# Performance work log

Hardware: AMD Instinct MI355X
Metric: run time of the kernel (lower is better)

## Reference

```python
import jax, jax.numpy as jnp
import numpy as np

INPUT_DIM = 512
D_KQ = 64
D_V = 64
SEQ = 8192


def setup_inputs() -> dict:
    key = jax.random.key(0)
    k_x, k_q, k_k, k_v = jax.random.split(key, 4)
    x = jax.random.normal(k_x, (SEQ, INPUT_DIM), dtype=jnp.float32)
    # Original uses torch.rand (uniform [0,1)) for the parameters.
    W_query = jax.random.uniform(k_q, (INPUT_DIM, D_KQ), dtype=jnp.float32)
    W_key = jax.random.uniform(k_k, (INPUT_DIM, D_KQ), dtype=jnp.float32)
    W_value = jax.random.uniform(k_v, (INPUT_DIM, D_V), dtype=jnp.float32)
    return {"x": x, "W_query": W_query, "W_key": W_key, "W_value": W_value}


def reference(x, W_query, W_key, W_value):
    # Full-recompute path of AttentionOptimized: single-head attention.
    Q = x @ W_query          # [T, d_kq]
    K = x @ W_key            # [T, d_kq]
    V = x @ W_value          # [T, d_v]
    scale = jnp.asarray(D_KQ, x.dtype) ** 0.5
    scores = Q @ K.T         # [T, T]
    attn = jax.nn.softmax(scores / scale, axis=-1)
    return attn @ V          # [T, d_v]
```

## Files before the change

kernel.cpp:

```cpp
#include <hip/hip_runtime.h>
#include <hip/hip_bf16.h>
#include <math.h>

#define SEQ 8192
#define DIN 512
#define DH  64
#define SG  8
#define CHUNK (SEQ / SG)
#define BK  64
#define NIT (CHUNK / BK)
#define LDK 64
#define SXP 516

typedef float f32x4 __attribute__((ext_vector_type(4)));
typedef short short8 __attribute__((ext_vector_type(8)));
typedef ushort us4 __attribute__((ext_vector_type(4)));

static __device__ __forceinline__ ushort bf16_of(float v) {
  __hip_bfloat16 h = __float2bfloat16(v);
  return *reinterpret_cast<ushort*>(&h);
}
static __device__ __forceinline__ float f_of_bf16(ushort u) {
  __hip_bfloat16 h;
  *reinterpret_cast<ushort*>(&h) = u;
  return __bfloat162float(h);
}
static __device__ __forceinline__ f32x4 mfma16(short8 a, short8 b, f32x4 c) {
  return __builtin_amdgcn_mfma_f32_16x16x32_bf16(a, b, c, 0, 0, 0);
}
static __device__ __forceinline__ uint pack_bf16(float a, float b) {
  __hip_bfloat162 h2 = __float22bfloat162_rn(make_float2(a, b));
  return *reinterpret_cast<uint*>(&h2);
}
static __device__ __forceinline__ int slot_of(int p) {
  return ((((p >> 2) & 1) * 2 + (p >> 5)) << 4) | (((p >> 3) & 3) << 2) | (p & 3);
}
static __device__ __forceinline__ int swz(int row, int col) {
  return col ^ ((row & 7) << 3);
}

__global__ __launch_bounds__(256, 2) void pgemm_kernel(
    const float* __restrict__ x,  const float* __restrict__ Wq,
    const float* __restrict__ Wk, const float* __restrict__ Wv,
    ushort* __restrict__ Qh, ushort* __restrict__ Ql,
    ushort* __restrict__ Kh, ushort* __restrict__ Kl,
    ushort* __restrict__ Vt) {
  __shared__ float sx[16][SXP];
  float* mb = &sx[0][0];

  const int tid = threadIdx.x;
  const int wv = tid >> 6, lane = tid & 63;
  const int ln = lane & 15, qd = lane >> 4;
  const int rb = blockIdx.x * 16;

  {
    const float4* xg = reinterpret_cast<const float4*>(x + (size_t)rb * DIN);
#pragma unroll
    for (int j = 0; j < 8; ++j) {
      const int idx = tid + 256 * j;
      const int row = idx >> 7;
      const int col = (idx & 127) * 4;
      *reinterpret_cast<float4*>(&sx[row][col]) = xg[idx];
    }
  }
  __syncthreads();

  f32x4 acc[3][4];
#pragma unroll
  for (int m = 0; m < 3; ++m)
#pragma unroll
    for (int nt = 0; nt < 4; ++nt)
#pragma unroll
      for (int i = 0; i < 4; ++i) acc[m][nt][i] = 0.f;

  const int kb = wv * 128;
  const int wbase = (kb + qd * 8) * 64 + ln;

  float wf[2][32];
#define LDW(kt_, m_, buf_)                                                     \
  do {                                                                         \
    const float* W_ = ((m_) == 0) ? Wq : (((m_) == 1) ? Wk : Wv);              \
    const int o_ = wbase + (kt_) * 32 * 64;                                    \
    _Pragma("unroll") for (int nt = 0; nt < 4; ++nt)                           \
      _Pragma("unroll") for (int j = 0; j < 8; ++j)                            \
        wf[buf_][nt * 8 + j] = W_[o_ + j * 64 + nt * 16];                      \
  } while (0)

  LDW(0, 0, 0);
#pragma unroll
  for (int kt = 0; kt < 4; ++kt) {
    const int k0 = kb + kt * 32;
    float xs[8];
    *reinterpret_cast<float4*>(xs) =
        *reinterpret_cast<const float4*>(&sx[ln][k0 + qd * 8]);
    *reinterpret_cast<float4*>(xs + 4) =
        *reinterpret_cast<const float4*>(&sx[ln][k0 + qd * 8 + 4]);
    ushort ah[8] __attribute__((aligned(16)));
    ushort al[8] __attribute__((aligned(16)));
#pragma unroll
    for (int j = 0; j < 8; ++j) {
      const ushort h = bf16_of(xs[j]);
      ah[j] = h;
      al[j] = bf16_of(xs[j] - f_of_bf16(h));
    }
    const short8 Ah = *reinterpret_cast<short8*>(ah);
    const short8 Al = *reinterpret_cast<short8*>(al);
#pragma unroll
    for (int m = 0; m < 3; ++m) {
      const int g = kt * 3 + m;
      const int buf = g & 1;
      if (g < 11) {
        const int gn = g + 1;
        LDW(gn / 3, gn % 3, buf ^ 1);
      }
      const float scale = (m == 0) ? 0.125f * 1.44269504088896f : 1.0f;
#pragma unroll
      for (int nt = 0; nt < 4; ++nt) {
        ushort bh8[8] __attribute__((aligned(16)));
        ushort bl8[8] __attribute__((aligned(16)));
#pragma unroll
        for (int j = 0; j < 8; ++j) {
          const float v = wf[buf][nt * 8 + j] * scale;
          const ushort h = bf16_of(v);
          bh8[j] = h;
          bl8[j] = bf16_of(v - f_of_bf16(h));
        }
        const short8 bh = *reinterpret_cast<short8*>(bh8);
        const short8 bl = *reinterpret_cast<short8*>(bl8);
        acc[m][nt] = mfma16(Ah, bh, acc[m][nt]);
        acc[m][nt] = mfma16(Ah, bl, acc[m][nt]);
        acc[m][nt] = mfma16(Al, bh, acc[m][nt]);
      }
    }
  }
#undef LDW

  const int eidx = (qd * 4) * 64 + ln;
  __syncthreads();
  if (wv >= 2) {
    float* b = mb + (size_t)(wv - 2) * 3072;
#pragma unroll
    for (int m = 0; m < 3; ++m)
#pragma unroll
      for (int nt = 0; nt < 4; ++nt)
#pragma unroll
        for (int r = 0; r < 4; ++r)
          b[m * 1024 + eidx + r * 64 + nt * 16] = acc[m][nt][r];
  }
  __syncthreads();
  if (wv < 2) {
    const float* b = mb + (size_t)wv * 3072;
#pragma unroll
    for (int m = 0; m < 3; ++m)
#pragma unroll
      for (int nt = 0; nt < 4; ++nt)
#pragma unroll
        for (int r = 0; r < 4; ++r)
          acc[m][nt][r] += b[m * 1024 + eidx + r * 64 + nt * 16];
  }
  __syncthreads();
  if (wv == 1) {
#pragma unroll
    for (int m = 0; m < 3; ++m)
#pragma unroll
      for (int nt = 0; nt < 4; ++nt)
#pragma unroll
        for (int r = 0; r < 4; ++r)
          mb[m * 1024 + eidx + r * 64 + nt * 16] = acc[m][nt][r];
  }
  __syncthreads();
  if (wv == 0) {
#pragma unroll
    for (int m = 0; m < 3; ++m)
#pragma unroll
      for (int nt = 0; nt < 4; ++nt)
#pragma unroll
        for (int r = 0; r < 4; ++r)
          acc[m][nt][r] += mb[m * 1024 + eidx + r * 64 + nt * 16];

#pragma unroll
    for (int m = 0; m < 2; ++m) {
      ushort* H = (m == 0) ? Qh : Kh;
      ushort* L = (m == 0) ? Ql : Kl;
#pragma unroll
      for (int nt = 0; nt < 4; ++nt)
#pragma unroll
        for (int r = 0; r < 4; ++r) {
          const float v = acc[m][nt][r];
          const int row = rb + qd * 4 + r;
          const int col = nt * 16 + ln;
          const ushort h = bf16_of(v);
          H[(size_t)row * DH + col] = h;
          L[(size_t)row * DH + col] = bf16_of(v - f_of_bf16(h));
        }
    }
#pragma unroll
    for (int nt = 0; nt < 4; ++nt) {
      ushort vp[4] __attribute__((aligned(8)));
#pragma unroll
      for (int r = 0; r < 4; ++r) vp[r] = bf16_of(acc[2][nt][r]);
      *reinterpret_cast<us4*>(Vt + (size_t)(nt * 16 + ln) * SEQ + rb + qd * 4) =
          *reinterpret_cast<us4*>(vp);
    }
  }
}

__global__ __launch_bounds__(256, 2) void flash_kernel(
    const ushort* __restrict__ Qh, const ushort* __restrict__ Ql,
    const ushort* __restrict__ Kh, const ushort* __restrict__ Kl,
    const ushort* __restrict__ Vt,
    ushort* __restrict__ Opart, float* __restrict__ Mpart,
    float* __restrict__ Lpart) {
  __shared__ __attribute__((aligned(16))) ushort sKh[3][BK][LDK];
  __shared__ __attribute__((aligned(16))) ushort sKl[3][BK][LDK];
  __shared__ __attribute__((aligned(16))) ushort sVt[3][DH][LDK];

  const int tid  = threadIdx.x;
  const int wv   = tid >> 6;
  const int lane = tid & 63;
  const int ln   = lane & 15;
  const int qd   = lane >> 4;
  const int bid  = blockIdx.x;
  const int sg   = bid & (SG - 1);
  const int qt   = bid >> 3;
  const int qrow0  = qt * 128 + wv * 32;
  const int k0base = sg * CHUNK;

  const int r0 = tid >> 3, g0 = (tid & 7) * 8;
  const int r1 = r0 + 32,  g1 = g0;
  const int sr0 = slot_of(r0), sr1 = slot_of(r1);

  const ushort one_u = (ln == 0) ? (ushort)0x3F80 : (ushort)0;
  short8 afr1;
#pragma unroll
  for (int j = 0; j < 8; ++j) afr1[j] = (short)one_u;

  short8 bqh[2][2], bql[2][2];
#pragma unroll
  for (int s = 0; s < 2; ++s)
#pragma unroll
    for (int kt = 0; kt < 2; ++kt) {
      bqh[s][kt] = *reinterpret_cast<const short8*>(
          Qh + (size_t)(qrow0 + s * 16 + ln) * DH + kt * 32 + qd * 8);
      bql[s][kt] = *reinterpret_cast<const short8*>(
          Ql + (size_t)(qrow0 + s * 16 + ln) * DH + kt * 32 + qd * 8);
    }

  f32x4 accO[2][4], accL[2];
  float m_run[2] = {-INFINITY, -INFINITY};
#pragma unroll
  for (int s = 0; s < 2; ++s) {
#pragma unroll
    for (int nt = 0; nt < 4; ++nt)
#pragma unroll
      for (int i = 0; i < 4; ++i) accO[s][nt][i] = 0.f;
#pragma unroll
    for (int i = 0; i < 4; ++i) accL[s][i] = 0.f;
  }
  const f32x4 z4 = {0.f, 0.f, 0.f, 0.f};

  f32x4 accSA[2][4], accSB[2][4];

  uint4 pk0, pk1, pl0, pl1, pv0, pv1;
#define LOAD_TILES(k0_)                                                        \
  do {                                                                         \
    pk0 = *reinterpret_cast<const uint4*>(Kh + (size_t)((k0_) + r0) * DH + g0);\
    pk1 = *reinterpret_cast<const uint4*>(Kh + (size_t)((k0_) + r1) * DH + g1);\
    pl0 = *reinterpret_cast<const uint4*>(Kl + (size_t)((k0_) + r0) * DH + g0);\
    pl1 = *reinterpret_cast<const uint4*>(Kl + (size_t)((k0_) + r1) * DH + g1);\
    pv0 = *reinterpret_cast<const uint4*>(Vt + (size_t)r0 * SEQ + (k0_) + g0); \
    pv1 = *reinterpret_cast<const uint4*>(Vt + (size_t)r1 * SEQ + (k0_) + g1); \
  } while (0)
#define STORE_TILES(b_)                                                        \
  do {                                                                         \
    *reinterpret_cast<uint4*>(&sKh[b_][sr0][swz(sr0, g0)]) = pk0;              \
    *reinterpret_cast<uint4*>(&sKh[b_][sr1][swz(sr1, g1)]) = pk1;              \
    *reinterpret_cast<uint4*>(&sKl[b_][sr0][swz(sr0, g0)]) = pl0;              \
    *reinterpret_cast<uint4*>(&sKl[b_][sr1][swz(sr1, g1)]) = pl1;              \
    *reinterpret_cast<uint4*>(&sVt[b_][r0][swz(r0, g0)])   = pv0;              \
    *reinterpret_cast<uint4*>(&sVt[b_][r1][swz(r1, g1)])   = pv1;              \
  } while (0)

#define QK_PHASE(ACC, b_)                                                      \
  do {                                                                         \
    _Pragma("unroll") for (int nt = 0; nt < 4; ++nt) {                         \
      const int kr = nt * 16 + ln;                                             \
      const short8 kh0 = *reinterpret_cast<const short8*>(                     \
          &sKh[b_][kr][swz(kr, qd * 8)]);                                      \
      const short8 kh1 = *reinterpret_cast<const short8*>(                     \
          &sKh[b_][kr][swz(kr, 32 + qd * 8)]);                                 \
      const short8 kl0 = *reinterpret_cast<const short8*>(                     \
          &sKl[b_][kr][swz(kr, qd * 8)]);                                      \
      const short8 kl1 = *reinterpret_cast<const short8*>(                     \
          &sKl[b_][kr][swz(kr, 32 + qd * 8)]);                                 \
      _Pragma("unroll") for (int s = 0; s < 2; ++s) {                          \
        ACC[s][nt] = mfma16(kh0, bqh[s][0], z4);                               \
        ACC[s][nt] = mfma16(kh1, bqh[s][1], ACC[s][nt]);                       \
        ACC[s][nt] = mfma16(kh0, bql[s][0], ACC[s][nt]);                       \
        ACC[s][nt] = mfma16(kh1, bql[s][1], ACC[s][nt]);                       \
        ACC[s][nt] = mfma16(kl0, bqh[s][0], ACC[s][nt]);                       \
        ACC[s][nt] = mfma16(kl1, bqh[s][1], ACC[s][nt]);                       \
      }                                                                        \
    }                                                                          \
  } while (0)

#define SMPV_PHASE(ACC, bc_)                                                   \
  do {                                                                         \
    uint pkd[2][4][2];                                                         \
    _Pragma("unroll") for (int s = 0; s < 2; ++s) {                            \
      float tmax = fmaxf(fmaxf(ACC[s][0][0], ACC[s][0][1]), ACC[s][0][2]);     \
      tmax = fmaxf(fmaxf(tmax, ACC[s][0][3]), ACC[s][1][0]);                   \
      tmax = fmaxf(fmaxf(tmax, ACC[s][1][1]), ACC[s][1][2]);                   \
      tmax = fmaxf(fmaxf(tmax, ACC[s][1][3]), ACC[s][2][0]);                   \
      tmax = fmaxf(fmaxf(tmax, ACC[s][2][1]), ACC[s][2][2]);                   \
      tmax = fmaxf(fmaxf(tmax, ACC[s][2][3]), ACC[s][3][0]);                   \
      tmax = fmaxf(fmaxf(tmax, ACC[s][3][1]), ACC[s][3][2]);                   \
      tmax = fmaxf(tmax, ACC[s][3][3]);                                        \
      tmax = fmaxf(tmax, __shfl_xor(tmax, 16));                                \
      tmax = fmaxf(tmax, __shfl_xor(tmax, 32));                                \
      if (tmax > m_run[s] + 8.f) {       \
        const float mnew  = fmaxf(m_run[s], tmax);                             \
        const float alpha = exp2f(m_run[s] - mnew);                            \
        m_run[s] = mnew;                                                       \
        _Pragma("unroll") for (int nt = 0; nt < 4; ++nt)                       \
          _Pragma("unroll") for (int i = 0; i < 4; ++i)                        \
            accO[s][nt][i] *= alpha;                                           \
        accL[s][0] *= alpha;                                                   \
      }                                                                        \
      const float mr = m_run[s];                                               \
      _Pragma("unroll") for (int nt = 0; nt < 4; ++nt) {                       \
        pkd[s][nt][0] = pack_bf16(exp2f(ACC[s][nt][0] - mr),                   \
                                  exp2f(ACC[s][nt][1] - mr));                  \
        pkd[s][nt][1] = pack_bf16(exp2f(ACC[s][nt][2] - mr),                   \
                                  exp2f(ACC[s][nt][3] - mr));                  \
      }                                                                        \
    }                                                                          \
    _Pragma("unroll") for (int kt2 = 0; kt2 < 2; ++kt2) {                      \
      short8 pfrag[2];                                                         \
      _Pragma("unroll") for (int s = 0; s < 2; ++s) {                          \
        uint4 du;                                                              \
        du.x = pkd[s][kt2][0];                                                 \
        du.y = pkd[s][kt2][1];                                                 \
        du.z = pkd[s][kt2 + 2][0];                                             \
        du.w = pkd[s][kt2 + 2][1];                                             \
        pfrag[s] = *reinterpret_cast<short8*>(&du);                            \
      }                                                                        \
      _Pragma("unroll") for (int nt2 = 0; nt2 < 4; ++nt2) {                    \
        const int vr = nt2 * 16 + ln;                                          \
        const short8 vA = *reinterpret_cast<const short8*>(                    \
            &sVt[bc_][vr][swz(vr, kt2 * 32 + qd * 8)]);                        \
        accO[0][nt2] = mfma16(vA, pfrag[0], accO[0][nt2]);                     \
        accO[1][nt2] = mfma16(vA, pfrag[1], accO[1][nt2]);                     \
      }                                                                        \
      accL[0] = mfma16(afr1, pfrag[0], accL[0]);                               \
      accL[1] = mfma16(afr1, pfrag[1], accL[1]);                               \
    }                                                                          \
  } while (0)

  LOAD_TILES(k0base);
  STORE_TILES(0);
  LOAD_TILES(k0base + BK);
  __syncthreads();
  QK_PHASE(accSA, 0);
  STORE_TILES(1);
  LOAD_TILES(k0base + 2 * BK);
  __syncthreads();

  int bc = 0, bn = 1, bs = 2;
#define BODY(ACC_CUR, ACC_NXT, t_)                                             \
  do {                                                                         \
    if ((t_) + 1 < NIT) QK_PHASE(ACC_NXT, bn);          \
    SMPV_PHASE(ACC_CUR, bc);                        \
    if ((t_) + 2 < NIT) STORE_TILES(bs);                                       \
    if ((t_) + 3 < NIT) LOAD_TILES(k0base + ((t_) + 3) * BK);                  \
    if ((t_) + 1 < NIT) __syncthreads();                                       \
    const int tb_ = bc; bc = bn; bn = bs; bs = tb_;                            \
  } while (0)

  for (int t = 0; t < NIT; t += 2) {
    BODY(accSA, accSB, t);
    BODY(accSB, accSA, t + 1);
  }
#undef BODY
#undef QK_PHASE
#undef SMPV_PHASE
#undef LOAD_TILES
#undef STORE_TILES

#pragma unroll
  for (int s = 0; s < 2; ++s) {
    const int qrow = qrow0 + s * 16 + ln;
    ushort* Ob = Opart + ((size_t)sg * SEQ + qrow) * DH;
#pragma unroll
    for (int nt = 0; nt < 4; ++nt) {
      ushort op[4] __attribute__((aligned(8)));
#pragma unroll
      for (int r = 0; r < 4; ++r) op[r] = bf16_of(accO[s][nt][r]);
      *reinterpret_cast<us4*>(Ob + nt * 16 + qd * 4) =
          *reinterpret_cast<us4*>(op);
    }
    if (qd == 0) {
      Mpart[(size_t)sg * SEQ + qrow] = m_run[s];
      Lpart[(size_t)sg * SEQ + qrow] = accL[s][0];
    }
  }
}

__global__ __launch_bounds__(256) void merge_kernel(
    const ushort* __restrict__ Opart, const float* __restrict__ Mpart,
    const float* __restrict__ Lpart, float* __restrict__ out) {
  const int idx = blockIdx.x * 256 + threadIdx.x;
  const int row = idx >> 4;
  const int c4  = (idx & 15) * 4;

  float m[SG];
  float M = -INFINITY;
#pragma unroll
  for (int i = 0; i < SG; ++i) {
    m[i] = Mpart[(size_t)i * SEQ + row];
    M = fmaxf(M, m[i]);
  }
  float L = 0.f;
  float a0 = 0.f, a1 = 0.f, a2 = 0.f, a3 = 0.f;
#pragma unroll
  for (int i = 0; i < SG; ++i) {
    const float w = exp2f(m[i] - M);
    L += w * Lpart[(size_t)i * SEQ + row];
    const us4 o = *reinterpret_cast<const us4*>(
        Opart + ((size_t)i * SEQ + row) * DH + c4);
    a0 += w * f_of_bf16(o[0]);
    a1 += w * f_of_bf16(o[1]);
    a2 += w * f_of_bf16(o[2]);
    a3 += w * f_of_bf16(o[3]);
  }
  const float rL = 1.0f / L;
  float4 res = make_float4(a0 * rL, a1 * rL, a2 * rL, a3 * rL);
  *reinterpret_cast<float4*>(out + (size_t)row * DH + c4) = res;
}

extern "C" void kernel_launch(void* const* d_in, const int* in_sizes, int n_in,
                              void* d_out, int out_size, void* d_ws, size_t ws_size,
                              hipStream_t stream) {
  const float* x  = (const float*)d_in[0];
  const float* Wq = (const float*)d_in[1];
  const float* Wk = (const float*)d_in[2];
  const float* Wv = (const float*)d_in[3];
  float* out = (float*)d_out;

  const size_t S64 = (size_t)SEQ * DH;
  ushort* Qh = (ushort*)d_ws;
  ushort* Ql = Qh + S64;
  ushort* Kh = Ql + S64;
  ushort* Kl = Kh + S64;
  ushort* Vt = Kl + S64;
  ushort* Op = Vt + S64;
  float*  Mp = (float*)(Op + (size_t)SG * S64);
  float*  Lp = Mp + (size_t)SG * SEQ;

  pgemm_kernel<<<SEQ / 16, 256, 0, stream>>>(x, Wq, Wk, Wv, Qh, Ql, Kh, Kl, Vt);
  flash_kernel<<<(SEQ / 128) * SG, 256, 0, stream>>>(Qh, Ql, Kh, Kl, Vt, Op, Mp, Lp);
  merge_kernel<<<(SEQ * 16) / 256, 256, 0, stream>>>(Op, Mp, Lp, out);
}
```

Baseline: 129.7 us.

## Fully unroll attention pipeline, reorder stores before compute, use lighter barriers

Fully unrolls the 16-iteration K/V tile loop with compile-time buffer indices (mod 3) in place of rotating runtime indices. In each step the LDS store of tile t+2 and the global load of tile t+3 now come before the QK and softmax·PV compute, rather than after. __syncthreads is replaced by an explicit lgkmcnt wait plus s_barrier, and the first barrier before tile 1's store is removed. The aim is better overlap of memory traffic with MFMA work and lower barrier and indexing overhead, at the cost of larger code and possible LDS hazards if the triple-buffer ordering is wrong.

After: 129.7 us. Within noise of the previous version (+0.0%).

```diff
diff --git a/kernel.cpp b/kernel.cpp
--- a/kernel.cpp
+++ b/kernel.cpp
@@ -37,6 +37,11 @@
 }
 static __device__ __forceinline__ int swz(int row, int col) {
   return col ^ ((row & 7) << 3);
+}
+
+static __device__ __forceinline__ void bar_lgkm() {
+  asm volatile("s_waitcnt lgkmcnt(0)" ::: "memory");
+  __builtin_amdgcn_s_barrier();
 }
 
 __global__ __launch_bounds__(256, 2) void pgemm_kernel(
@@ -360,27 +365,36 @@
   LOAD_TILES(k0base);
   STORE_TILES(0);
   LOAD_TILES(k0base + BK);
-  __syncthreads();
-  QK_PHASE(accSA, 0);
   STORE_TILES(1);
   LOAD_TILES(k0base + 2 * BK);
-  __syncthreads();
-
-  int bc = 0, bn = 1, bs = 2;
-#define BODY(ACC_CUR, ACC_NXT, t_)                                             \
-  do {                                                                         \
-    if ((t_) + 1 < NIT) QK_PHASE(ACC_NXT, bn);          \
-    SMPV_PHASE(ACC_CUR, bc);                        \
-    if ((t_) + 2 < NIT) STORE_TILES(bs);                                       \
-    if ((t_) + 3 < NIT) LOAD_TILES(k0base + ((t_) + 3) * BK);                  \
-    if ((t_) + 1 < NIT) __syncthreads();                                       \
-    const int tb_ = bc; bc = bn; bn = bs; bs = tb_;                            \
-  } while (0)
-
-  for (int t = 0; t < NIT; t += 2) {
-    BODY(accSA, accSB, t);
-    BODY(accSB, accSA, t + 1);
-  }
+  bar_lgkm();
+  QK_PHASE(accSA, 0);
+
+#define BODY(t_, AC, AN)                                                       \
+  do {                                                                         \
+    if ((t_) <= NIT - 3) STORE_TILES(((t_) + 2) % 3);                          \
+    if ((t_) <= NIT - 4) LOAD_TILES(k0base + ((t_) + 3) * BK);                 \
+    if ((t_) <= NIT - 2) QK_PHASE(AN, ((t_) + 1) % 3);                         \
+    SMPV_PHASE(AC, (t_) % 3);                                                  \
+    if ((t_) <= NIT - 2) bar_lgkm();                                           \
+  } while (0)
+
+  BODY(0,  accSA, accSB);
+  BODY(1,  accSB, accSA);
+  BODY(2,  accSA, accSB);
+  BODY(3,  accSB, accSA);
+  BODY(4,  accSA, accSB);
+  BODY(5,  accSB, accSA);
+  BODY(6,  accSA, accSB);
+  BODY(7,  accSB, accSA);
+  BODY(8,  accSA, accSB);
+  BODY(9,  accSB, accSA);
+  BODY(10, accSA, accSB);
+  BODY(11, accSB, accSA);
+  BODY(12, accSA, accSB);
+  BODY(13, accSB, accSA);
+  BODY(14, accSA, accSB);
+  BODY(15, accSB, accSA);
 #undef BODY
 #undef QK_PHASE
 #undef SMPV_PHASE
```
